# Kernel optimization log

Measured on AMD Instinct MI355X. Metric: run time of the kernel, lower is better.

The kernel has to match this reference:

```python
import jax, jax.numpy as jnp
import numpy as np


def setup_inputs() -> dict:
    key = jax.random.key(0)
    k1, k2, k3, k4 = jax.random.split(key, 4)
    B, T, C, H = 8, 2048, 1024, 64
    x = jax.random.normal(k1, (B, T, C), dtype=jnp.float32)
    Wq = jax.random.normal(k2, (C, H), dtype=jnp.float32) * (C ** -0.5)
    Wk = jax.random.normal(k3, (C, H), dtype=jnp.float32) * (C ** -0.5)
    Wv = jax.random.normal(k4, (C, H), dtype=jnp.float32) * (C ** -0.5)
    return {"x": x, "Wq": Wq, "Wk": Wk, "Wv": Wv}


def reference(x, Wq, Wk, Wv):
    # x: [B,T,C]; Wq/Wk/Wv: [C,H] (nn.Linear bias=False => x @ W)
    B, T, C = x.shape
    H = Wq.shape[-1]
    q = jnp.einsum('btc,ch->bth', x, Wq)
    k = jnp.einsum('btc,ch->bth', x, Wk)
    v = jnp.einsum('btc,ch->bth', x, Wv)
    scale = H ** -0.5
    att = jnp.einsum('bqh,bkh->bqk', q, k) * scale  # [B,T,T]
    causal = jnp.tril(jnp.ones((T, T), dtype=bool))
    att = jnp.where(causal, att, -jnp.inf)
    att = jax.nn.softmax(att, axis=-1)
    out = jnp.einsum('bqk,bkh->bqh', att, v)  # [B,T,H]
    return out
```

## Files before the change

### kernel.cpp

```cpp
#include <hip/hip_runtime.h>
#include <hip/hip_bf16.h>
#include <math.h>

#define BB 8
#define TT 2048
#define CC 1024
#define HH 64
#define BT (BB * TT)

typedef __attribute__((ext_vector_type(8))) short short8;
typedef __attribute__((ext_vector_type(4))) float floatx4;

static __device__ inline ushort f2bf(float f) {
    __hip_bfloat16 h = __float2bfloat16(f);
    return *reinterpret_cast<ushort*>(&h);
}
static __device__ inline unsigned int f2bf2(float lo, float hi) {
    __hip_bfloat162 h = __float22bfloat162_rn(make_float2(lo, hi));
    return *reinterpret_cast<unsigned int*>(&h);
}
static __device__ inline float bf2f(ushort u) {
    union { unsigned int i; float f; } c;
    c.i = ((unsigned int)u) << 16;
    return c.f;
}

__global__ __launch_bounds__(256) void wprep_kernel(
    const float* __restrict__ Wq, const float* __restrict__ Wk,
    const float* __restrict__ Wv, ushort* __restrict__ WbT)
{
    __shared__ float ws_[64 * 65];
    const int m  = blockIdx.x >> 4;
    const int kb = (blockIdx.x & 15) * 64;
    const float* W = (m == 0) ? Wq : (m == 1) ? Wk : Wv;
    const int t  = threadIdx.x;
    const int lr = t >> 4, lc = (t & 15) * 4;
    #pragma unroll
    for (int i = 0; i < 4; ++i) {
        const int row = lr + i * 16;
        float4 v = *(const float4*)&W[(size_t)(kb + row) * HH + lc];
        ws_[row * 65 + lc + 0] = v.x; ws_[row * 65 + lc + 1] = v.y;
        ws_[row * 65 + lc + 2] = v.z; ws_[row * 65 + lc + 3] = v.w;
    }
    __syncthreads();
    const int n = t & 63, kseg = t >> 6;
    union { ushort s[16]; uint4 q[2]; } u;
    #pragma unroll
    for (int j = 0; j < 16; ++j)
        u.s[j] = f2bf(ws_[(kseg * 16 + j) * 65 + n]);
    ushort* dst = &WbT[(size_t)(m * 64 + n) * 1024 + kb + kseg * 16];
    *(uint4*)&dst[0] = u.q[0];
    *(uint4*)&dst[8] = u.q[1];
}

__global__ __launch_bounds__(256) void qkv_kernel(
    const float* __restrict__ x, const ushort* __restrict__ WbT,
    ushort* __restrict__ qb, ushort* __restrict__ kbS, ushort* __restrict__ vS)
{
    const int row0 = blockIdx.x * 32;
    const int t    = threadIdx.x;
    const int w    = t >> 6;
    const int lane = t & 63;
    const int l16  = lane & 15;
    const int quad = lane >> 4;
    const int ct0  = w * 3;

    floatx4 acc[2][3];
    #pragma unroll
    for (int mt = 0; mt < 2; ++mt)
        #pragma unroll
        for (int c = 0; c < 3; ++c) acc[mt][c] = (floatx4){0.f, 0.f, 0.f, 0.f};

    const float* xr0 = &x[(size_t)(row0 + l16) * CC + quad * 8];
    const float* xr1 = xr0 + 16 * CC;

    float4 xc[4][2], xn[4][2];
    #pragma unroll
    for (int mt = 0; mt < 2; ++mt)
        #pragma unroll
        for (int p = 0; p < 2; ++p) {
            const float* src = (mt ? xr1 : xr0) + p * 32;
            xc[mt * 2 + p][0] = *(const float4*)&src[0];
            xc[mt * 2 + p][1] = *(const float4*)&src[4];
        }

    short8 bfr[2][3], bnx[2][3];
    #pragma unroll
    for (int p = 0; p < 2; ++p)
        #pragma unroll
        for (int c = 0; c < 3; ++c)
            bfr[p][c] = *(const short8*)&WbT[(size_t)((ct0 + c) * 16 + l16) * 1024
                                             + p * 32 + quad * 8];

    for (int it = 0; it < 16; ++it) {
        if (it < 15) {
            const int kn = (it + 1) * 64;
            #pragma unroll
            for (int mt = 0; mt < 2; ++mt)
                #pragma unroll
                for (int p = 0; p < 2; ++p) {
                    const float* src = (mt ? xr1 : xr0) + kn + p * 32;
                    xn[mt * 2 + p][0] = *(const float4*)&src[0];
                    xn[mt * 2 + p][1] = *(const float4*)&src[4];
                }
            #pragma unroll
            for (int p = 0; p < 2; ++p)
                #pragma unroll
                for (int c = 0; c < 3; ++c)
                    bnx[p][c] = *(const short8*)&WbT[(size_t)((ct0 + c) * 16 + l16) * 1024
                                                     + kn + p * 32 + quad * 8];
        }

        short8 afr[2][2];
        #pragma unroll
        for (int mt = 0; mt < 2; ++mt)
            #pragma unroll
            for (int p = 0; p < 2; ++p) {
                const float4 a = xc[mt * 2 + p][0];
                const float4 b = xc[mt * 2 + p][1];
                union { unsigned int u[4]; short8 s; } cv;
                cv.u[0] = f2bf2(a.x, a.y); cv.u[1] = f2bf2(a.z, a.w);
                cv.u[2] = f2bf2(b.x, b.y); cv.u[3] = f2bf2(b.z, b.w);
                afr[mt][p] = cv.s;
            }

        __builtin_amdgcn_s_setprio(1);
        #pragma unroll
        for (int p = 0; p < 2; ++p)
            #pragma unroll
            for (int c = 0; c < 3; ++c) {
                acc[0][c] = __builtin_amdgcn_mfma_f32_16x16x32_bf16(afr[0][p], bfr[p][c], acc[0][c], 0, 0, 0);
                acc[1][c] = __builtin_amdgcn_mfma_f32_16x16x32_bf16(afr[1][p], bfr[p][c], acc[1][c], 0, 0, 0);
            }
        __builtin_amdgcn_s_setprio(0);

        #pragma unroll
        for (int i = 0; i < 4; ++i) { xc[i][0] = xn[i][0]; xc[i][1] = xn[i][1]; }
        #pragma unroll
        for (int p = 0; p < 2; ++p)
            #pragma unroll
            for (int c = 0; c < 3; ++c) bfr[p][c] = bnx[p][c];
    }

    const int half = (row0 >> 5) & 1;
    const size_t tile = (size_t)(row0 >> 6) * 4096;
    #pragma unroll
    for (int c = 0; c < 3; ++c) {
        const int ct    = ct0 + c;
        const int mtype = ct >> 2;
        const int n0    = (ct & 3) * 16;
        #pragma unroll
        for (int mt = 0; mt < 2; ++mt) {
            const int row = row0 + mt * 16 + quad * 4;
            if (mtype == 0) {
                #pragma unroll
                for (int reg = 0; reg < 4; ++reg)
                    qb[(size_t)(row + reg) * HH + n0 + l16] = f2bf(acc[mt][c][reg] * 0.125f);
            } else if (mtype == 1) {
                const int cP    = half * 2 + mt;
                const int pP    = (ct & 3) >> 1;
                const int quadP = ((ct & 3) * 2 + (l16 >> 3)) & 3;
                const int jP    = l16 & 7;
                const int ub    = (cP * 2 + pP) * 64 + quadP * 16;
                #pragma unroll
                for (int reg = 0; reg < 4; ++reg)
                    kbS[tile + (size_t)(ub + quad * 4 + reg) * 8 + jP] = f2bf(acc[mt][c][reg]);
            } else {
                const int cp2 = (ct & 3) * 2 + half;
                #pragma unroll
                for (int reg = 0; reg < 4; ++reg) {
                    const int rq    = quad * 4 + reg;
                    const int quadP = mt * 2 + (rq >> 3);
                    vS[tile + (size_t)(cp2 * 64 + quadP * 16 + l16) * 8 + (rq & 7)] = f2bf(acc[mt][c][reg]);
                }
            }
        }
    }
}

__global__ __launch_bounds__(256) void attn_kernel(
    const ushort* __restrict__ qb, const ushort* __restrict__ kbS,
    const ushort* __restrict__ vS, ushort* __restrict__ Opart,
    float* __restrict__ ml)
{
    __shared__ __align__(16) ushort P[4][16 * 72];

    const int t    = threadIdx.x;
    const int w    = t >> 6;
    const int lane = t & 63;
    const int l16  = lane & 15;
    const int quad = lane >> 4;

    const int b   = blockIdx.x & 7;
    const int idx = blockIdx.x >> 3;
    int qt, part, np;
    if (idx < 32)      { qt = 31 - (idx >> 2); part = idx & 3; np = 4; }
    else if (idx < 56) { const int u = idx - 32; const int g = u / 3;
                         qt = 23 - g; part = u - g * 3; np = 3; }
    else if (idx < 72) { const int u = idx - 56; qt = 15 - (u >> 1); part = u & 1; np = 2; }
    else               { qt = 7 - (idx - 72); part = 0; np = 1; }
    const int ntiles = qt + 1;
    const int ktb = (part * ntiles) / np;
    const int kte = ((part + 1) * ntiles) / np;

    const ushort* ktile0 = kbS + (size_t)(b * 32) * 4096;
    const ushort* vtile0 = vS  + (size_t)(b * 32) * 4096;

    short8 qf[2];
    {
        const ushort* qrow = qb + ((size_t)b * TT + qt * 64 + w * 16) * HH;
        qf[0] = *(const short8*)&qrow[l16 * HH + quad * 8];
        qf[1] = *(const short8*)&qrow[l16 * HH + 32 + quad * 8];
    }
    short8 ones;
    #pragma unroll
    for (int i = 0; i < 8; ++i) ones[i] = (short)0x3F80;

    floatx4 o[4], osum;
    #pragma unroll
    for (int c = 0; c < 4; ++c) o[c] = (floatx4){0.f, 0.f, 0.f, 0.f};
    osum = (floatx4){0.f, 0.f, 0.f, 0.f};

    ushort* Pw = &P[w][0];

    for (int kt = ktb; kt < kte; ++kt) {
        const ushort* kg = ktile0 + (size_t)kt * 4096;
        const ushort* vg = vtile0 + (size_t)kt * 4096;

        short8 kf[4][2];
        #pragma unroll
        for (int c = 0; c < 4; ++c)
            #pragma unroll
            for (int p = 0; p < 2; ++p)
                kf[c][p] = *(const short8*)&kg[(size_t)(((c * 2 + p) * 64) + lane) * 8];

        floatx4 s[4];
        #pragma unroll
        for (int c = 0; c < 4; ++c) s[c] = (floatx4){0.f, 0.f, 0.f, 0.f};
        __builtin_amdgcn_s_setprio(1);
        #pragma unroll
        for (int c = 0; c < 4; ++c)
            #pragma unroll
            for (int p = 0; p < 2; ++p)
                s[c] = __builtin_amdgcn_mfma_f32_16x16x32_bf16(kf[c][p], qf[p], s[c], 0, 0, 0);
        __builtin_amdgcn_s_setprio(0);

        short8 vf[4][2];
        #pragma unroll
        for (int c = 0; c < 4; ++c)
            #pragma unroll
            for (int p = 0; p < 2; ++p)
                vf[c][p] = *(const short8*)&vg[(size_t)(((c * 2 + p) * 64) + lane) * 8];

        if (kt == ntiles - 1) {
            const int key0 = kt * 64 + quad * 4;
            const int qrow = qt * 64 + w * 16 + l16;
            #pragma unroll
            for (int c = 0; c < 4; ++c)
                #pragma unroll
                for (int reg = 0; reg < 4; ++reg)
                    if (key0 + c * 16 + reg > qrow) s[c][reg] = -1e30f;
        }

        #pragma unroll
        for (int c = 0; c < 4; ++c) {
            uint2 u;
            u.x = f2bf2(__expf(s[c][0]), __expf(s[c][1]));
            u.y = f2bf2(__expf(s[c][2]), __expf(s[c][3]));
            *(uint2*)&Pw[l16 * 72 + c * 16 + quad * 4] = u;
        }

        short8 pf[2];
        pf[0] = *(const short8*)&Pw[l16 * 72 + quad * 8];
        pf[1] = *(const short8*)&Pw[l16 * 72 + 32 + quad * 8];

        __builtin_amdgcn_s_setprio(1);
        #pragma unroll
        for (int p = 0; p < 2; ++p) {
            #pragma unroll
            for (int c = 0; c < 4; ++c)
                o[c] = __builtin_amdgcn_mfma_f32_16x16x32_bf16(pf[p], vf[c][p], o[c], 0, 0, 0);
            osum = __builtin_amdgcn_mfma_f32_16x16x32_bf16(pf[p], ones, osum, 0, 0, 0);
        }
        __builtin_amdgcn_s_setprio(0);
    }

    const size_t ub = (size_t)blockIdx.x * 4096;
    const int rbase = w * 16 + quad * 4;
    #pragma unroll
    for (int c = 0; c < 4; ++c) {
        uint2 u;
        u.x = f2bf2(o[c][0], o[c][1]);
        u.y = f2bf2(o[c][2], o[c][3]);
        *(uint2*)&Opart[ub + (size_t)(c * 16 + l16) * 64 + rbase] = u;
    }
    if (l16 == 0) {
        #pragma unroll
        for (int reg = 0; reg < 4; ++reg)
            ml[(size_t)blockIdx.x * 64 + rbase + reg] = osum[reg];
    }
}

__global__ __launch_bounds__(256) void merge_kernel(
    const ushort* __restrict__ Opart, const float* __restrict__ ml,
    float* __restrict__ out)
{
    const int t    = threadIdx.x;
    const int gw   = blockIdx.x * 4 + (t >> 6);
    const int lane = t & 63;
    const int b    = gw >> 8;
    const int v    = gw & 255;
    const int qt   = v >> 3;
    const int oct  = v & 7;

    int base, np;
    if (qt >= 24)      { base = (31 - qt) * 4;      np = 4; }
    else if (qt >= 16) { base = 32 + (23 - qt) * 3; np = 3; }
    else if (qt >= 8)  { base = 56 + (15 - qt) * 2; np = 2; }
    else               { base = 72 + (7 - qt);      np = 1; }

    float* obase = out + ((size_t)b * TT + qt * 64) * HH;

    #pragma unroll
    for (int rg = 0; rg < 2; ++rg) {
        const int row0 = oct * 8 + rg * 4;
        float dx = 0.f, dy = 0.f, dz = 0.f, dw = 0.f;
        float ax = 0.f, ay = 0.f, az = 0.f, aw = 0.f;
        for (int p = 0; p < np; ++p) {
            const int unit = (base + p) * 8 + b;
            float4 d = *(const float4*)&ml[(size_t)unit * 64 + row0];
            dx += d.x; dy += d.y; dz += d.z; dw += d.w;
            ushort4 ov = *(const ushort4*)&Opart[(size_t)unit * 4096 + lane * 64 + row0];
            ax += bf2f(ov.x); ay += bf2f(ov.y); az += bf2f(ov.z); aw += bf2f(ov.w);
        }
        obase[(size_t)(row0 + 0) * HH + lane] = ax / dx;
        obase[(size_t)(row0 + 1) * HH + lane] = ay / dy;
        obase[(size_t)(row0 + 2) * HH + lane] = az / dz;
        obase[(size_t)(row0 + 3) * HH + lane] = aw / dw;
    }
}

extern "C" void kernel_launch(void* const* d_in, const int* in_sizes, int n_in,
                              void* d_out, int out_size, void* d_ws, size_t ws_size,
                              hipStream_t stream)
{
    (void)in_sizes; (void)n_in; (void)out_size; (void)ws_size;
    const float* x  = (const float*)d_in[0];
    const float* Wq = (const float*)d_in[1];
    const float* Wk = (const float*)d_in[2];
    const float* Wv = (const float*)d_in[3];
    float* outp = (float*)d_out;

    char* base = (char*)d_ws;
    ushort* WbT   = (ushort*)(base);
    ushort* qbuf  = (ushort*)(base + 393216);
    ushort* kbS   = qbuf + (size_t)BT * HH;
    ushort* vSb   = kbS + (size_t)BT * HH;
    ushort* Opart = vSb + (size_t)BT * HH;
    float*  ml    = (float*)((char*)Opart + (size_t)640 * 4096 * 2);

    wprep_kernel<<<dim3(48),  256, 0, stream>>>(Wq, Wk, Wv, WbT);
    qkv_kernel  <<<dim3(512), 256, 0, stream>>>(x, WbT, qbuf, kbS, vSb);
    attn_kernel <<<dim3(640), 256, 0, stream>>>(qbuf, kbS, vSb, Opart, ml);
    merge_kernel<<<dim3(512), 256, 0, stream>>>(Opart, ml, outp);
}
```

Baseline: 158.6 us.

## Halve QKV projection row tile and stage bf16 x tile through swizzled LDS

The QKV projection kernel now handles 16 rows per block instead of 32, doubling the grid to 1024 blocks. Each thread loads one float4 of x per k-step, converts it to bf16 and writes it to a double-buffered, XOR-swizzled shared-memory tile that all waves read back as MFMA A fragments. Before, every wave loaded and converted the full x tile itself. This cuts redundant global x loads and conversions and raises occupancy, at the cost of one barrier per k-step and re-reading the weight fragments twice as often across blocks.

```diff
diff --git a/kernel.cpp b/kernel.cpp
--- a/kernel.cpp
+++ b/kernel.cpp
@@ -57,7 +57,9 @@
     const float* __restrict__ x, const ushort* __restrict__ WbT,
     ushort* __restrict__ qb, ushort* __restrict__ kbS, ushort* __restrict__ vS)
 {
-    const int row0 = blockIdx.x * 32;
+    __shared__ __align__(16) ushort As[2][1024];
+
+    const int row0 = blockIdx.x * 16;
     const int t    = threadIdx.x;
     const int w    = t >> 6;
     const int lane = t & 63;
@@ -65,24 +67,21 @@
     const int quad = lane >> 4;
     const int ct0  = w * 3;
 
-    floatx4 acc[2][3];
-    #pragma unroll
-    for (int mt = 0; mt < 2; ++mt)
-        #pragma unroll
-        for (int c = 0; c < 3; ++c) acc[mt][c] = (floatx4){0.f, 0.f, 0.f, 0.f};
-
-    const float* xr0 = &x[(size_t)(row0 + l16) * CC + quad * 8];
-    const float* xr1 = xr0 + 16 * CC;
-
-    float4 xc[4][2], xn[4][2];
-    #pragma unroll
-    for (int mt = 0; mt < 2; ++mt)
-        #pragma unroll
-        for (int p = 0; p < 2; ++p) {
-            const float* src = (mt ? xr1 : xr0) + p * 32;
-            xc[mt * 2 + p][0] = *(const float4*)&src[0];
-            xc[mt * 2 + p][1] = *(const float4*)&src[4];
-        }
+    const int srow = t >> 4, sseg = t & 15;
+    const int sp = sseg >> 3, squad = (sseg >> 1) & 3, shalf = sseg & 1;
+    const int widx = (((sp * 64 + srow * 4 + squad) * 8) + shalf * 4)
+                     ^ ((srow & 7) << 3);
+    const float* xsrc = &x[(size_t)(row0 + srow) * CC + sseg * 4];
+
+    const int ridx0 = ((l16 * 4 + quad) * 8)       ^ ((l16 & 7) << 3);
+    const int ridx1 = ((64 + l16 * 4 + quad) * 8)  ^ ((l16 & 7) << 3);
+
+    floatx4 acc[3];
+    #pragma unroll
+    for (int c = 0; c < 3; ++c) acc[c] = (floatx4){0.f, 0.f, 0.f, 0.f};
+
+    float4 xc = *(const float4*)&xsrc[0];
+    float4 xn;
 
     short8 bfr[2][3], bnx[2][3];
     #pragma unroll
@@ -93,16 +92,15 @@
                                              + p * 32 + quad * 8];
 
     for (int it = 0; it < 16; ++it) {
+        uint2 uq;
+        uq.x = f2bf2(xc.x, xc.y);
+        uq.y = f2bf2(xc.z, xc.w);
+        *(uint2*)&As[it & 1][widx] = uq;
+        __syncthreads();
+
         if (it < 15) {
+            xn = *(const float4*)&xsrc[(it + 1) * 64];
             const int kn = (it + 1) * 64;
-            #pragma unroll
-            for (int mt = 0; mt < 2; ++mt)
-                #pragma unroll
-                for (int p = 0; p < 2; ++p) {
-                    const float* src = (mt ? xr1 : xr0) + kn + p * 32;
-                    xn[mt * 2 + p][0] = *(const float4*)&src[0];
-                    xn[mt * 2 + p][1] = *(const float4*)&src[4];
-                }
             #pragma unroll
             for (int p = 0; p < 2; ++p)
                 #pragma unroll
@@ -111,68 +109,53 @@
                                                      + kn + p * 32 + quad * 8];
         }
 
-        short8 afr[2][2];
-        #pragma unroll
-        for (int mt = 0; mt < 2; ++mt)
-            #pragma unroll
-            for (int p = 0; p < 2; ++p) {
-                const float4 a = xc[mt * 2 + p][0];
-                const float4 b = xc[mt * 2 + p][1];
-                union { unsigned int u[4]; short8 s; } cv;
-                cv.u[0] = f2bf2(a.x, a.y); cv.u[1] = f2bf2(a.z, a.w);
-                cv.u[2] = f2bf2(b.x, b.y); cv.u[3] = f2bf2(b.z, b.w);
-                afr[mt][p] = cv.s;
-            }
+        short8 a0 = *(const short8*)&As[it & 1][ridx0];
+        short8 a1 = *(const short8*)&As[it & 1][ridx1];
 
         __builtin_amdgcn_s_setprio(1);
         #pragma unroll
+        for (int c = 0; c < 3; ++c) {
+            acc[c] = __builtin_amdgcn_mfma_f32_16x16x32_bf16(a0, bfr[0][c], acc[c], 0, 0, 0);
+            acc[c] = __builtin_amdgcn_mfma_f32_16x16x32_bf16(a1, bfr[1][c], acc[c], 0, 0, 0);
+        }
+        __builtin_amdgcn_s_setprio(0);
+
+        xc = xn;
+        #pragma unroll
         for (int p = 0; p < 2; ++p)
             #pragma unroll
-            for (int c = 0; c < 3; ++c) {
-                acc[0][c] = __builtin_amdgcn_mfma_f32_16x16x32_bf16(afr[0][p], bfr[p][c], acc[0][c], 0, 0, 0);
-                acc[1][c] = __builtin_amdgcn_mfma_f32_16x16x32_bf16(afr[1][p], bfr[p][c], acc[1][c], 0, 0, 0);
-            }
-        __builtin_amdgcn_s_setprio(0);
-
-        #pragma unroll
-        for (int i = 0; i < 4; ++i) { xc[i][0] = xn[i][0]; xc[i][1] = xn[i][1]; }
-        #pragma unroll
-        for (int p = 0; p < 2; ++p)
-            #pragma unroll
             for (int c = 0; c < 3; ++c) bfr[p][c] = bnx[p][c];
     }
 
     const int half = (row0 >> 5) & 1;
+    const int mt   = (row0 >> 4) & 1;
     const size_t tile = (size_t)(row0 >> 6) * 4096;
     #pragma unroll
     for (int c = 0; c < 3; ++c) {
         const int ct    = ct0 + c;
         const int mtype = ct >> 2;
         const int n0    = (ct & 3) * 16;
-        #pragma unroll
-        for (int mt = 0; mt < 2; ++mt) {
-            const int row = row0 + mt * 16 + quad * 4;
-            if (mtype == 0) {
-                #pragma unroll
-                for (int reg = 0; reg < 4; ++reg)
-                    qb[(size_t)(row + reg) * HH + n0 + l16] = f2bf(acc[mt][c][reg] * 0.125f);
-            } else if (mtype == 1) {
-                const int cP    = half * 2 + mt;
-                const int pP    = (ct & 3) >> 1;
-                const int quadP = ((ct & 3) * 2 + (l16 >> 3)) & 3;
-                const int jP    = l16 & 7;
-                const int ub    = (cP * 2 + pP) * 64 + quadP * 16;
-                #pragma unroll
-                for (int reg = 0; reg < 4; ++reg)
-                    kbS[tile + (size_t)(ub + quad * 4 + reg) * 8 + jP] = f2bf(acc[mt][c][reg]);
-            } else {
-                const int cp2 = (ct & 3) * 2 + half;
-                #pragma unroll
-                for (int reg = 0; reg < 4; ++reg) {
-                    const int rq    = quad * 4 + reg;
-                    const int quadP = mt * 2 + (rq >> 3);
-                    vS[tile + (size_t)(cp2 * 64 + quadP * 16 + l16) * 8 + (rq & 7)] = f2bf(acc[mt][c][reg]);
-                }
+        const int row   = row0 + quad * 4;
+        if (mtype == 0) {
+            #pragma unroll
+            for (int reg = 0; reg < 4; ++reg)
+                qb[(size_t)(row + reg) * HH + n0 + l16] = f2bf(acc[c][reg] * 0.125f);
+        } else if (mtype == 1) {
+            const int cP    = half * 2 + mt;
+            const int pP    = (ct & 3) >> 1;
+            const int quadP = ((ct & 3) * 2 + (l16 >> 3)) & 3;
+            const int jP    = l16 & 7;
+            const int ub    = (cP * 2 + pP) * 64 + quadP * 16;
+            #pragma unroll
+            for (int reg = 0; reg < 4; ++reg)
+                kbS[tile + (size_t)(ub + quad * 4 + reg) * 8 + jP] = f2bf(acc[c][reg]);
+        } else {
+            const int cp2 = (ct & 3) * 2 + half;
+            #pragma unroll
+            for (int reg = 0; reg < 4; ++reg) {
+                const int rq    = quad * 4 + reg;
+                const int quadP = mt * 2 + (rq >> 3);
+                vS[tile + (size_t)(cp2 * 64 + quadP * 16 + l16) * 8 + (rq & 7)] = f2bf(acc[c][reg]);
             }
         }
     }
@@ -359,8 +342,8 @@
     ushort* Opart = vSb + (size_t)BT * HH;
     float*  ml    = (float*)((char*)Opart + (size_t)640 * 4096 * 2);
 
-    wprep_kernel<<<dim3(48),  256, 0, stream>>>(Wq, Wk, Wv, WbT);
-    qkv_kernel  <<<dim3(512), 256, 0, stream>>>(x, WbT, qbuf, kbS, vSb);
-    attn_kernel <<<dim3(640), 256, 0, stream>>>(qbuf, kbS, vSb, Opart, ml);
-    merge_kernel<<<dim3(512), 256, 0, stream>>>(Opart, ml, outp);
-}
+    wprep_kernel<<<dim3(48),   256, 0, stream>>>(Wq, Wk, Wv, WbT);
+    qkv_kernel  <<<dim3(1024), 256, 0, stream>>>(x, WbT, qbuf, kbS, vSb);
+    attn_kernel <<<dim3(640),  256, 0, stream>>>(qbuf, kbS, vSb, Opart, ml);
+    merge_kernel<<<dim3(512),  256, 0, stream>>>(Opart, ml, outp);
+}
```

After: 154.5 us. 1.03x faster.

## Stage x tiles into LDS via global_load_lds with a 4-buffer pipeline

Applied to the files above, without the earlier changes.

The QKV projection kernel now loads x with direct global-to-LDS loads into a swizzled four-slot shared-memory ring, prefetching three K-steps ahead. Previously each of the four waves loaded the same x rows redundantly into registers. Weight fragments are double-buffered two steps ahead, and the loop is fully unrolled with hand-tuned vmcnt waits and barriers. This cuts redundant global traffic and register pressure, but adds LDS usage (32KB), per-iteration barriers, and fragile wait counts that must match the exact number of outstanding loads.

```diff
diff --git a/kernel.cpp b/kernel.cpp
--- a/kernel.cpp
+++ b/kernel.cpp
@@ -23,6 +23,12 @@
     union { unsigned int i; float f; } c;
     c.i = ((unsigned int)u) << 16;
     return c.f;
+}
+static __device__ inline void gl_ldsf(const float* g, float* l) {
+    __builtin_amdgcn_global_load_lds(
+        (const __attribute__((address_space(1))) unsigned int*)g,
+        (__attribute__((address_space(3))) unsigned int*)l,
+        16, 0, 0);
 }
 
 __global__ __launch_bounds__(256) void wprep_kernel(
@@ -57,6 +63,8 @@
     const float* __restrict__ x, const ushort* __restrict__ WbT,
     ushort* __restrict__ qb, ushort* __restrict__ kbS, ushort* __restrict__ vS)
 {
+    __shared__ __align__(16) float Xs[4][2048];
+
     const int row0 = blockIdx.x * 32;
     const int t    = threadIdx.x;
     const int w    = t >> 6;
@@ -65,82 +73,91 @@
     const int quad = lane >> 4;
     const int ct0  = w * 3;
 
+    const int d0 = lane & 1, d1 = (lane >> 1) & 1, d2 = (lane >> 2) & 1, d3 = (lane >> 3) & 1;
+    const int quads = (d1 ^ d2 ^ d3) + 2 * (d2 ^ d3);
+    const int hh    = d0 ^ d1 ^ d2 ^ d3;
+    const int kof   = (w >> 1) * 32 + quads * 8 + hh * 4;
+    const int rowA  = (w & 1) * 16 + ((lane >> 3) & 7);
+    const float* srcA = &x[(size_t)(row0 + rowA) * CC + kof];
+    const float* srcB = srcA + (size_t)8 * CC;
+
+    int off[4][2];
+    #pragma unroll
+    for (int f = 0; f < 4; ++f) {
+        const int Sr = f * 64 + l16 * 4 + quad;
+        const int sw = (Sr & 7) << 4;
+        off[f][0] = (Sr * 32) ^ sw;
+        off[f][1] = (Sr * 32 + 16) ^ sw;
+    }
+
     floatx4 acc[2][3];
     #pragma unroll
     for (int mt = 0; mt < 2; ++mt)
         #pragma unroll
         for (int c = 0; c < 3; ++c) acc[mt][c] = (floatx4){0.f, 0.f, 0.f, 0.f};
 
-    const float* xr0 = &x[(size_t)(row0 + l16) * CC + quad * 8];
-    const float* xr1 = xr0 + 16 * CC;
-
-    float4 xc[4][2], xn[4][2];
-    #pragma unroll
-    for (int mt = 0; mt < 2; ++mt)
-        #pragma unroll
-        for (int p = 0; p < 2; ++p) {
-            const float* src = (mt ? xr1 : xr0) + p * 32;
-            xc[mt * 2 + p][0] = *(const float4*)&src[0];
-            xc[mt * 2 + p][1] = *(const float4*)&src[4];
-        }
-
-    short8 bfr[2][3], bnx[2][3];
-    #pragma unroll
-    for (int p = 0; p < 2; ++p)
-        #pragma unroll
-        for (int c = 0; c < 3; ++c)
-            bfr[p][c] = *(const short8*)&WbT[(size_t)((ct0 + c) * 16 + l16) * 1024
-                                             + p * 32 + quad * 8];
-
+    #define STAGE(buf, itx) do {                                   \
+        gl_ldsf(srcA + (itx) * 64, &Xs[buf][w * 512]);             \
+        gl_ldsf(srcB + (itx) * 64, &Xs[buf][w * 512 + 256]);       \
+    } while (0)
+
+    STAGE(0, 0); STAGE(1, 1); STAGE(2, 2);
+    asm volatile("" ::: "memory");
+
+    short8 bW[2][2][3];
+    #pragma unroll
+    for (int s = 0; s < 2; ++s)
+        #pragma unroll
+        for (int p = 0; p < 2; ++p)
+            #pragma unroll
+            for (int c = 0; c < 3; ++c)
+                bW[s][p][c] = *(const short8*)&WbT[(size_t)((ct0 + c) * 16 + l16) * 1024
+                                                   + s * 64 + p * 32 + quad * 8];
+
+    #pragma unroll
     for (int it = 0; it < 16; ++it) {
-        if (it < 15) {
-            const int kn = (it + 1) * 64;
-            #pragma unroll
-            for (int mt = 0; mt < 2; ++mt)
-                #pragma unroll
-                for (int p = 0; p < 2; ++p) {
-                    const float* src = (mt ? xr1 : xr0) + kn + p * 32;
-                    xn[mt * 2 + p][0] = *(const float4*)&src[0];
-                    xn[mt * 2 + p][1] = *(const float4*)&src[4];
-                }
+        if (it == 0)       asm volatile("s_waitcnt vmcnt(16)" ::: "memory");
+        else if (it < 14)  asm volatile("s_waitcnt vmcnt(22)" ::: "memory");
+        else if (it == 14) asm volatile("s_waitcnt vmcnt(20)" ::: "memory");
+        else               asm volatile("s_waitcnt vmcnt(12)" ::: "memory");
+        __builtin_amdgcn_s_barrier();
+
+        if (it + 3 < 16) STAGE((it + 3) & 3, it + 3);
+        asm volatile("" ::: "memory");
+
+        const char* bufc = (const char*)&Xs[it & 3][0];
+        short8 a[4];
+        #pragma unroll
+        for (int f = 0; f < 4; ++f) {
+            float4 lo = *(const float4*)(bufc + off[f][0]);
+            float4 hi = *(const float4*)(bufc + off[f][1]);
+            union { unsigned int u[4]; short8 s; } cv;
+            cv.u[0] = f2bf2(lo.x, lo.y); cv.u[1] = f2bf2(lo.z, lo.w);
+            cv.u[2] = f2bf2(hi.x, hi.y); cv.u[3] = f2bf2(hi.z, hi.w);
+            a[f] = cv.s;
+        }
+
+        __builtin_amdgcn_s_setprio(1);
+        #pragma unroll
+        for (int c = 0; c < 3; ++c) {
+            acc[0][c] = __builtin_amdgcn_mfma_f32_16x16x32_bf16(a[0], bW[it & 1][0][c], acc[0][c], 0, 0, 0);
+            acc[1][c] = __builtin_amdgcn_mfma_f32_16x16x32_bf16(a[1], bW[it & 1][0][c], acc[1][c], 0, 0, 0);
+            acc[0][c] = __builtin_amdgcn_mfma_f32_16x16x32_bf16(a[2], bW[it & 1][1][c], acc[0][c], 0, 0, 0);
+            acc[1][c] = __builtin_amdgcn_mfma_f32_16x16x32_bf16(a[3], bW[it & 1][1][c], acc[1][c], 0, 0, 0);
+        }
+        __builtin_amdgcn_s_setprio(0);
+
+        if (it + 2 < 16) {
+            const int kn = (it + 2) * 64;
             #pragma unroll
             for (int p = 0; p < 2; ++p)
                 #pragma unroll
                 for (int c = 0; c < 3; ++c)
-                    bnx[p][c] = *(const short8*)&WbT[(size_t)((ct0 + c) * 16 + l16) * 1024
-                                                     + kn + p * 32 + quad * 8];
-        }
-
-        short8 afr[2][2];
-        #pragma unroll
-        for (int mt = 0; mt < 2; ++mt)
-            #pragma unroll
-            for (int p = 0; p < 2; ++p) {
-                const float4 a = xc[mt * 2 + p][0];
-                const float4 b = xc[mt * 2 + p][1];
-                union { unsigned int u[4]; short8 s; } cv;
-                cv.u[0] = f2bf2(a.x, a.y); cv.u[1] = f2bf2(a.z, a.w);
-                cv.u[2] = f2bf2(b.x, b.y); cv.u[3] = f2bf2(b.z, b.w);
-                afr[mt][p] = cv.s;
-            }
-
-        __builtin_amdgcn_s_setprio(1);
-        #pragma unroll
-        for (int p = 0; p < 2; ++p)
-            #pragma unroll
-            for (int c = 0; c < 3; ++c) {
-                acc[0][c] = __builtin_amdgcn_mfma_f32_16x16x32_bf16(afr[0][p], bfr[p][c], acc[0][c], 0, 0, 0);
-                acc[1][c] = __builtin_amdgcn_mfma_f32_16x16x32_bf16(afr[1][p], bfr[p][c], acc[1][c], 0, 0, 0);
-            }
-        __builtin_amdgcn_s_setprio(0);
-
-        #pragma unroll
-        for (int i = 0; i < 4; ++i) { xc[i][0] = xn[i][0]; xc[i][1] = xn[i][1]; }
-        #pragma unroll
-        for (int p = 0; p < 2; ++p)
-            #pragma unroll
-            for (int c = 0; c < 3; ++c) bfr[p][c] = bnx[p][c];
-    }
+                    bW[it & 1][p][c] = *(const short8*)&WbT[(size_t)((ct0 + c) * 16 + l16) * 1024
+                                                            + kn + p * 32 + quad * 8];
+        }
+    }
+    #undef STAGE
 
     const int half = (row0 >> 5) & 1;
     const size_t tile = (size_t)(row0 >> 6) * 4096;
```

New measurement: 136.0 us. 14.3% less time.
